# Kernel optimization log

Hardware: AMD Instinct MI355X
Metric: run time of the kernel (lower is better)

Reference implementation:

```python
import jax, jax.numpy as jnp
import numpy as np

NCE_T = 0.07   # opt.nce_T
EPS = 1e-8     # torch CosineSimilarity eps
DIAG_FILL = -10.0

N, D = 8192, 256

def setup_inputs() -> dict:
    key = jax.random.key(0)
    kq, kk = jax.random.split(key)
    feat_q = jax.random.normal(kq, (N, D), dtype=jnp.float32)
    feat_k = jax.random.normal(kk, (N, D), dtype=jnp.float32)
    return {"feat_q": feat_q, "feat_k": feat_k}

def reference(feat_q, feat_k):
    # feat_k is detached in the original
    feat_k = jax.lax.stop_gradient(feat_k)
    nq = jnp.linalg.norm(feat_q, axis=-1)            # [N]
    nk = jnp.linalg.norm(feat_k, axis=-1)            # [N]
    # positive cosine similarity (paired rows)
    l_pos = jnp.sum(feat_q * feat_k, axis=-1) / jnp.maximum(nq * nk, EPS)  # [N]
    # full N x N cosine similarity via GEMM (torch does a broadcasted version)
    sim = (feat_q @ feat_k.T) / jnp.maximum(nq[:, None] * nk[None, :], EPS)  # [N,N]
    # mask self-similarities with -10.0 BEFORE dividing by temperature
    diag = jnp.eye(sim.shape[0], dtype=bool)
    l_neg = jnp.where(diag, DIAG_FILL, sim)
    out = jnp.concatenate([l_pos[:, None], l_neg], axis=1) / NCE_T  # [N, N+1]
    # cross-entropy vs target class 0, reduction='none'
    loss = jax.scipy.special.logsumexp(out, axis=1) - out[:, 0]     # [N]
    return loss
```

## Files before the change

kernel.cpp:

```cpp
#include <hip/hip_runtime.h>
#include <stdint.h>
#include <math.h>

#define NROWS 8192
#define DDIM  256
#define BM    128
#define BN    128
#define GJ    8
#define COLS_PER_GROUP (NROWS / GJ)

constexpr float INV_T  = 1.0f / 0.07f;
constexpr float LOG2E  = 1.44269504f;
constexpr float K1     = INV_T * LOG2E;

typedef __bf16 bf16x8 __attribute__((ext_vector_type(8)));
typedef float  f32x4  __attribute__((ext_vector_type(4)));

__device__ __forceinline__ void async_copy16(const uint16_t* g, uint16_t* l) {
    __builtin_amdgcn_global_load_lds(
        (const __attribute__((address_space(1))) uint32_t*)g,
        (__attribute__((address_space(3))) uint32_t*)l, 16, 0, 0);
}

__device__ inline uint16_t f2bf(float f) {
    uint32_t u = __float_as_uint(f);
    u += 0x7fffu + ((u >> 16) & 1u);
    return (uint16_t)(u >> 16);
}

__global__ __launch_bounds__(256) void norm_convert_kernel(
    const float* __restrict__ fq, const float* __restrict__ fk,
    uint16_t* __restrict__ qb, uint16_t* __restrict__ kb)
{
    const int wave = threadIdx.x >> 6;
    const int lane = threadIdx.x & 63;
    const int row  = blockIdx.x * 4 + wave;

    const float* src; uint16_t* dstb;
    if (row < NROWS) {
        src = fq + (size_t)row * DDIM; dstb = qb + (size_t)row * DDIM;
    } else {
        int r = row - NROWS;
        src = fk + (size_t)r * DDIM; dstb = kb + (size_t)r * DDIM;
    }

    float4 v = ((const float4*)src)[lane];
    float ss = v.x*v.x + v.y*v.y + v.z*v.z + v.w*v.w;
    #pragma unroll
    for (int m = 1; m < 64; m <<= 1) ss += __shfl_xor(ss, m, 64);
    float r = rsqrtf(ss);

    ushort4 o;
    o.x = f2bf(v.x * r); o.y = f2bf(v.y * r); o.z = f2bf(v.z * r); o.w = f2bf(v.w * r);
    ((ushort4*)dstb)[lane] = o;
}

__global__ __launch_bounds__(256, 2) void nce_main_kernel(
    const uint16_t* __restrict__ qb, const uint16_t* __restrict__ kb,
    float* __restrict__ lpT, float* __restrict__ gpl)
{
    __shared__ __align__(16) uint16_t lds_q[BM * DDIM];
    __shared__ __align__(16) uint16_t lds_k[2 * BN * 32];

    const int tid    = threadIdx.x;
    const int wave   = tid >> 6;
    const int lane   = tid & 63;
    const int quad   = lane >> 4;
    const int lanelo = lane & 15;
    const int wr     = wave >> 1;
    const int wc     = wave & 1;
    const int rowBase      = blockIdx.x * BM;
    const int colGroupBase = blockIdx.y * COLS_PER_GROUP;

    #pragma unroll
    for (int i = 0; i < 16; ++i) {
        int S   = (wave * 16 + i) * 64 + lane;
        int row = S >> 5;
        int ch  = (S & 31) ^ (row & 31);
        async_copy16(qb + (size_t)(rowBase + row) * DDIM + ch * 8,
                     lds_q + (size_t)(wave * 16 + i) * 512);
    }

    int kS0   = wave * 128 + lane;
    int krow0 = kS0 >> 2;
    int kch0  = (lane & 3) ^ (krow0 & 3);
    int krow1 = (kS0 + 64) >> 2;
    int kch1  = (lane & 3) ^ (krow1 & 3);
    const uint16_t* kbase0 = kb + (size_t)(colGroupBase + krow0) * DDIM + kch0 * 8;
    const uint16_t* kbase1 = kb + (size_t)(colGroupBase + krow1) * DDIM + kch1 * 8;
    uint16_t* kl0 = lds_k + wave * 1024;

    async_copy16(kbase0, kl0);
    async_copy16(kbase1, kl0 + 512);
    __syncthreads();

    int rq[4], rq31[4];
    #pragma unroll
    for (int mt = 0; mt < 4; ++mt) {
        rq[mt]   = wr * 64 + mt * 16 + lanelo;
        rq31[mt] = rq[mt] & 31;
    }
    int bvoff[4];
    #pragma unroll
    for (int nt = 0; nt < 4; ++nt) {
        int rk = wc * 64 + nt * 16 + lanelo;
        bvoff[nt] = rk * 32 + (quad ^ (rk & 3)) * 8;
    }

    float l_run[16];
    #pragma unroll
    for (int i = 0; i < 16; ++i) l_run[i] = 0.f;

    for (int jt = 0; jt < 8; ++jt) {
        const int colT = colGroupBase + jt * BN;

        f32x4 acc[4][4];
        #pragma unroll
        for (int mt = 0; mt < 4; ++mt)
            #pragma unroll
            for (int nt = 0; nt < 4; ++nt)
                acc[mt][nt] = (f32x4){0.f, 0.f, 0.f, 0.f};

        #pragma unroll
        for (int kk = 0; kk < 8; ++kk) {
            const int p    = (jt << 3) + kk;
            const int buf  = p & 1;
            const int nbuf = buf ^ 1;

            if (p < 63) {
                int np  = p + 1;
                int off = ((np >> 3) << 15) + ((np & 7) << 5);
                uint16_t* ld = lds_k + nbuf * 4096 + wave * 1024;
                async_copy16(kbase0 + off, ld);
                async_copy16(kbase1 + off, ld + 512);
            }

            bf16x8 av[4], bv[4];
            #pragma unroll
            for (int mt = 0; mt < 4; ++mt) {
                int chp = ((kk << 2) + quad) ^ rq31[mt];
                av[mt] = *(const bf16x8*)&lds_q[rq[mt] * 256 + chp * 8];
            }
            #pragma unroll
            for (int nt = 0; nt < 4; ++nt)
                bv[nt] = *(const bf16x8*)&lds_k[buf * 4096 + bvoff[nt]];
            #pragma unroll
            for (int mt = 0; mt < 4; ++mt)
                #pragma unroll
                for (int nt = 0; nt < 4; ++nt)
                    acc[mt][nt] = __builtin_amdgcn_mfma_f32_16x16x32_bf16(av[mt], bv[nt], acc[mt][nt], 0, 0, 0);

            __syncthreads();
        }

        int gcol[4];
        #pragma unroll
        for (int nt = 0; nt < 4; ++nt) gcol[nt] = colT + wc * 64 + nt * 16 + lanelo;
        #pragma unroll
        for (int mt = 0; mt < 4; ++mt) {
            #pragma unroll
            for (int rg = 0; rg < 4; ++rg) {
                int grow = rowBase + wr * 64 + mt * 16 + quad * 4 + rg;
                float s = 0.f;
                #pragma unroll
                for (int nt = 0; nt < 4; ++nt) {
                    float a = acc[mt][nt][rg];
                    float e = exp2f(fmaf(a, K1, -K1));
                    if (grow == gcol[nt]) { lpT[grow] = a * INV_T; e = 0.f; }
                    s += e;
                }
                l_run[mt * 4 + rg] += s;
            }
        }
    }

    #pragma unroll
    for (int i = 0; i < 16; ++i) {
        float v = l_run[i];
        v += __shfl_xor(v, 1, 64);
        v += __shfl_xor(v, 2, 64);
        v += __shfl_xor(v, 4, 64);
        v += __shfl_xor(v, 8, 64);
        l_run[i] = v;
    }
    float* pl = (float*)lds_k;
    if (lanelo == 0) {
        #pragma unroll
        for (int mt = 0; mt < 4; ++mt)
            #pragma unroll
            for (int rg = 0; rg < 4; ++rg) {
                int lr = wr * 64 + mt * 16 + quad * 4 + rg;
                pl[wc * 128 + lr] = l_run[mt * 4 + rg];
            }
    }
    __syncthreads();
    if (tid < 128) {
        float L = pl[tid] + pl[128 + tid];
        gpl[(size_t)blockIdx.y * NROWS + rowBase + tid] = L;
    }
}

__global__ __launch_bounds__(256) void finalize_kernel(
    const float* __restrict__ gpl, const float* __restrict__ lpT,
    float* __restrict__ out)
{
    int t = blockIdx.x * 256 + threadIdx.x;
    if (t >= NROWS) return;
    float L = 0.f;
    #pragma unroll
    for (int g = 0; g < GJ; ++g) L += gpl[g * NROWS + t];
    float lp = lpT[t];
    L += __expf(lp - INV_T);
    out[t] = INV_T + __logf(L) - lp;
}

extern "C" void kernel_launch(void* const* d_in, const int* in_sizes, int n_in,
                              void* d_out, int out_size, void* d_ws, size_t ws_size,
                              hipStream_t stream) {
    const float* fq = (const float*)d_in[0];
    const float* fk = (const float*)d_in[1];
    char* ws = (char*)d_ws;
    uint16_t* qb  = (uint16_t*)(ws);
    uint16_t* kb  = (uint16_t*)(ws + 4194304);
    float*    lpT = (float*)(ws + 8388608);
    float*    gpl = (float*)(ws + 8421376);

    norm_convert_kernel<<<(2 * NROWS) / 4, 256, 0, stream>>>(fq, fk, qb, kb);
    dim3 grid(NROWS / BM, GJ);
    nce_main_kernel<<<grid, 256, 0, stream>>>(qb, kb, lpT, gpl);
    finalize_kernel<<<NROWS / 256, 256, 0, stream>>>(gpl, lpT, (float*)d_out);
}
```

Baseline: 112.3 us.

## Keep Q tile in registers and deepen K pipeline to four LDS buffers

The Q operand fragments are loaded once from global memory into registers (128 VGPRs per lane) instead of being staged through a 64KB LDS tile and re-read every k-step. The K stream now uses a 4-buffer ring with a prefetch distance of 3, and a vmcnt wait plus a raw barrier replace the full __syncthreads. MFMA sections are also wrapped with s_setprio. This frees LDS, removes the A-side LDS reads and allows deeper latency hiding, but raises register pressure, which could cause spills or lower occupancy under launch_bounds(256,2).

```diff
diff --git a/kernel.cpp b/kernel.cpp
--- a/kernel.cpp
+++ b/kernel.cpp
@@ -59,8 +59,7 @@
     const uint16_t* __restrict__ qb, const uint16_t* __restrict__ kb,
     float* __restrict__ lpT, float* __restrict__ gpl)
 {
-    __shared__ __align__(16) uint16_t lds_q[BM * DDIM];
-    __shared__ __align__(16) uint16_t lds_k[2 * BN * 32];
+    __shared__ __align__(16) uint16_t lds_k[4 * BN * 32];
 
     const int tid    = threadIdx.x;
     const int wave   = tid >> 6;
@@ -72,13 +71,14 @@
     const int rowBase      = blockIdx.x * BM;
     const int colGroupBase = blockIdx.y * COLS_PER_GROUP;
 
-    #pragma unroll
-    for (int i = 0; i < 16; ++i) {
-        int S   = (wave * 16 + i) * 64 + lane;
-        int row = S >> 5;
-        int ch  = (S & 31) ^ (row & 31);
-        async_copy16(qb + (size_t)(rowBase + row) * DDIM + ch * 8,
-                     lds_q + (size_t)(wave * 16 + i) * 512);
+    bf16x8 aq[4][8];
+    #pragma unroll
+    for (int mt = 0; mt < 4; ++mt) {
+        const uint16_t* qrow =
+            qb + (size_t)(rowBase + wr * 64 + mt * 16 + lanelo) * DDIM + quad * 8;
+        #pragma unroll
+        for (int kk = 0; kk < 8; ++kk)
+            aq[mt][kk] = *(const bf16x8*)(qrow + kk * 32);
     }
 
     int kS0   = wave * 128 + lane;
@@ -88,18 +88,14 @@
     int kch1  = (lane & 3) ^ (krow1 & 3);
     const uint16_t* kbase0 = kb + (size_t)(colGroupBase + krow0) * DDIM + kch0 * 8;
     const uint16_t* kbase1 = kb + (size_t)(colGroupBase + krow1) * DDIM + kch1 * 8;
-    uint16_t* kl0 = lds_k + wave * 1024;
-
-    async_copy16(kbase0, kl0);
-    async_copy16(kbase1, kl0 + 512);
-    __syncthreads();
-
-    int rq[4], rq31[4];
-    #pragma unroll
-    for (int mt = 0; mt < 4; ++mt) {
-        rq[mt]   = wr * 64 + mt * 16 + lanelo;
-        rq31[mt] = rq[mt] & 31;
-    }
+
+    #pragma unroll
+    for (int p = 0; p < 3; ++p) {
+        uint16_t* ld = lds_k + (p << 12) + (wave << 10);
+        async_copy16(kbase0 + (p << 5), ld);
+        async_copy16(kbase1 + (p << 5), ld + 512);
+    }
+
     int bvoff[4];
     #pragma unroll
     for (int nt = 0; nt < 4; ++nt) {
@@ -123,34 +119,34 @@
 
         #pragma unroll
         for (int kk = 0; kk < 8; ++kk) {
-            const int p    = (jt << 3) + kk;
-            const int buf  = p & 1;
-            const int nbuf = buf ^ 1;
-
-            if (p < 63) {
-                int np  = p + 1;
-                int off = ((np >> 3) << 15) + ((np & 7) << 5);
-                uint16_t* ld = lds_k + nbuf * 4096 + wave * 1024;
+            const int p = (jt << 3) + kk;
+
+            asm volatile("s_waitcnt vmcnt(4)" ::: "memory");
+            __builtin_amdgcn_s_barrier();
+
+            {
+                const int np  = p + 3;
+                const int npm = np & 63;
+                const int off = ((npm >> 3) << 15) + ((npm & 7) << 5);
+                uint16_t* ld = lds_k + ((np & 3) << 12) + (wave << 10);
                 async_copy16(kbase0 + off, ld);
                 async_copy16(kbase1 + off, ld + 512);
             }
 
-            bf16x8 av[4], bv[4];
-            #pragma unroll
-            for (int mt = 0; mt < 4; ++mt) {
-                int chp = ((kk << 2) + quad) ^ rq31[mt];
-                av[mt] = *(const bf16x8*)&lds_q[rq[mt] * 256 + chp * 8];
-            }
+            bf16x8 bv[4];
+            const int bufo = (p & 3) << 12;
             #pragma unroll
             for (int nt = 0; nt < 4; ++nt)
-                bv[nt] = *(const bf16x8*)&lds_k[buf * 4096 + bvoff[nt]];
+                bv[nt] = *(const bf16x8*)&lds_k[bufo + bvoff[nt]];
+
+            __builtin_amdgcn_s_setprio(1);
             #pragma unroll
             for (int mt = 0; mt < 4; ++mt)
                 #pragma unroll
                 for (int nt = 0; nt < 4; ++nt)
-                    acc[mt][nt] = __builtin_amdgcn_mfma_f32_16x16x32_bf16(av[mt], bv[nt], acc[mt][nt], 0, 0, 0);
-
-            __syncthreads();
+                    acc[mt][nt] = __builtin_amdgcn_mfma_f32_16x16x32_bf16(
+                        aq[mt][kk], bv[nt], acc[mt][nt], 0, 0, 0);
+            __builtin_amdgcn_s_setprio(0);
         }
 
         int gcol[4];
@@ -183,6 +179,9 @@
         v += __shfl_xor(v, 8, 64);
         l_run[i] = v;
     }
+
+    __syncthreads();
+
     float* pl = (float*)lds_k;
     if (lanelo == 0) {
         #pragma unroll
```

Result: slower. 116.5 us (+3.7%).

## Fuse normalize, GEMM and finalize into one cooperative kernel with grid syncs

Applied to the files above, without the earlier changes.

Replaces the three-kernel sequence with a single cooperative launch: the blocks first normalize and convert rows to bf16, sync the whole grid, run the GEMM/logsumexp phase, sync again, then finalize the per-row loss. The aim is to remove two kernel launch gaps and their tail effects. It also changes the LDS XOR swizzle for the K tile to use (row>>1)&3, to cut bank conflicts on the B-fragment reads. It keeps the old three-kernel path as a fallback if the cooperative launch fails. Grid syncs add a barrier cost, and the 512-block grid must fit co-resident at two blocks per CU.

```diff
diff --git a/kernel.cpp b/kernel.cpp
--- a/kernel.cpp
+++ b/kernel.cpp
@@ -1,4 +1,5 @@
 #include <hip/hip_runtime.h>
+#include <hip/hip_cooperative_groups.h>
 #include <stdint.h>
 #include <math.h>
 
@@ -16,6 +17,8 @@
 typedef __bf16 bf16x8 __attribute__((ext_vector_type(8)));
 typedef float  f32x4  __attribute__((ext_vector_type(4)));
 
+namespace cg = cooperative_groups;
+
 __device__ __forceinline__ void async_copy16(const uint16_t* g, uint16_t* l) {
     __builtin_amdgcn_global_load_lds(
         (const __attribute__((address_space(1))) uint32_t*)g,
@@ -28,40 +31,22 @@
     return (uint16_t)(u >> 16);
 }
 
-__global__ __launch_bounds__(256) void norm_convert_kernel(
-    const float* __restrict__ fq, const float* __restrict__ fk,
-    uint16_t* __restrict__ qb, uint16_t* __restrict__ kb)
-{
-    const int wave = threadIdx.x >> 6;
-    const int lane = threadIdx.x & 63;
-    const int row  = blockIdx.x * 4 + wave;
-
-    const float* src; uint16_t* dstb;
-    if (row < NROWS) {
-        src = fq + (size_t)row * DDIM; dstb = qb + (size_t)row * DDIM;
-    } else {
-        int r = row - NROWS;
-        src = fk + (size_t)r * DDIM; dstb = kb + (size_t)r * DDIM;
-    }
-
+__device__ __forceinline__ void norm_row(const float* src, uint16_t* dstb, int lane) {
     float4 v = ((const float4*)src)[lane];
     float ss = v.x*v.x + v.y*v.y + v.z*v.z + v.w*v.w;
     #pragma unroll
     for (int m = 1; m < 64; m <<= 1) ss += __shfl_xor(ss, m, 64);
     float r = rsqrtf(ss);
-
     ushort4 o;
     o.x = f2bf(v.x * r); o.y = f2bf(v.y * r); o.z = f2bf(v.z * r); o.w = f2bf(v.w * r);
     ((ushort4*)dstb)[lane] = o;
 }
 
-__global__ __launch_bounds__(256, 2) void nce_main_kernel(
+__device__ __forceinline__ void gemm_phase(
     const uint16_t* __restrict__ qb, const uint16_t* __restrict__ kb,
-    float* __restrict__ lpT, float* __restrict__ gpl)
-{
-    __shared__ __align__(16) uint16_t lds_q[BM * DDIM];
-    __shared__ __align__(16) uint16_t lds_k[2 * BN * 32];
-
+    float* __restrict__ lpT, float* __restrict__ gpl,
+    uint16_t* lds_q, uint16_t* lds_k, int bx, int by)
+{
     const int tid    = threadIdx.x;
     const int wave   = tid >> 6;
     const int lane   = tid & 63;
@@ -69,8 +54,8 @@
     const int lanelo = lane & 15;
     const int wr     = wave >> 1;
     const int wc     = wave & 1;
-    const int rowBase      = blockIdx.x * BM;
-    const int colGroupBase = blockIdx.y * COLS_PER_GROUP;
+    const int rowBase      = bx * BM;
+    const int colGroupBase = by * COLS_PER_GROUP;
 
     #pragma unroll
     for (int i = 0; i < 16; ++i) {
@@ -83,9 +68,9 @@
 
     int kS0   = wave * 128 + lane;
     int krow0 = kS0 >> 2;
-    int kch0  = (lane & 3) ^ (krow0 & 3);
+    int kch0  = (lane & 3) ^ ((krow0 >> 1) & 3);
     int krow1 = (kS0 + 64) >> 2;
-    int kch1  = (lane & 3) ^ (krow1 & 3);
+    int kch1  = (lane & 3) ^ ((krow1 >> 1) & 3);
     const uint16_t* kbase0 = kb + (size_t)(colGroupBase + krow0) * DDIM + kch0 * 8;
     const uint16_t* kbase1 = kb + (size_t)(colGroupBase + krow1) * DDIM + kch1 * 8;
     uint16_t* kl0 = lds_k + wave * 1024;
@@ -104,7 +89,7 @@
     #pragma unroll
     for (int nt = 0; nt < 4; ++nt) {
         int rk = wc * 64 + nt * 16 + lanelo;
-        bvoff[nt] = rk * 32 + (quad ^ (rk & 3)) * 8;
+        bvoff[nt] = rk * 32 + (quad ^ ((lanelo >> 1) & 3)) * 8;
     }
 
     float l_run[16];
@@ -196,8 +181,71 @@
     __syncthreads();
     if (tid < 128) {
         float L = pl[tid] + pl[128 + tid];
-        gpl[(size_t)blockIdx.y * NROWS + rowBase + tid] = L;
-    }
+        gpl[(size_t)by * NROWS + rowBase + tid] = L;
+    }
+}
+
+__global__ __launch_bounds__(256, 2) void fused_kernel(
+    const float* __restrict__ fq, const float* __restrict__ fk,
+    uint16_t* __restrict__ qb, uint16_t* __restrict__ kb,
+    float* __restrict__ lpT, float* __restrict__ gpl,
+    float* __restrict__ out)
+{
+    __shared__ __align__(16) uint16_t lds_q[BM * DDIM];
+    __shared__ __align__(16) uint16_t lds_k[2 * BN * 32];
+
+    const int wave = threadIdx.x >> 6;
+    const int lane = threadIdx.x & 63;
+    const int flat = blockIdx.y * gridDim.x + blockIdx.x;
+
+    #pragma unroll
+    for (int i = 0; i < 8; ++i) {
+        int row = flat * 32 + wave * 8 + i;
+        if (row < NROWS) norm_row(fq + (size_t)row * DDIM, qb + (size_t)row * DDIM, lane);
+        else {
+            int r = row - NROWS;
+            norm_row(fk + (size_t)r * DDIM, kb + (size_t)r * DDIM, lane);
+        }
+    }
+
+    cg::this_grid().sync();
+
+    gemm_phase(qb, kb, lpT, gpl, lds_q, lds_k, blockIdx.x, blockIdx.y);
+
+    cg::this_grid().sync();
+
+    int t = flat * 16 + threadIdx.x;
+    if (threadIdx.x < 16) {
+        float L = 0.f;
+        #pragma unroll
+        for (int g = 0; g < GJ; ++g) L += gpl[g * NROWS + t];
+        float lp = lpT[t];
+        L += __expf(lp - INV_T);
+        out[t] = INV_T + __logf(L) - lp;
+    }
+}
+
+__global__ __launch_bounds__(256) void norm_convert_kernel(
+    const float* __restrict__ fq, const float* __restrict__ fk,
+    uint16_t* __restrict__ qb, uint16_t* __restrict__ kb)
+{
+    const int wave = threadIdx.x >> 6;
+    const int lane = threadIdx.x & 63;
+    const int row  = blockIdx.x * 4 + wave;
+    if (row < NROWS) norm_row(fq + (size_t)row * DDIM, qb + (size_t)row * DDIM, lane);
+    else {
+        int r = row - NROWS;
+        norm_row(fk + (size_t)r * DDIM, kb + (size_t)r * DDIM, lane);
+    }
+}
+
+__global__ __launch_bounds__(256, 2) void nce_main_kernel(
+    const uint16_t* __restrict__ qb, const uint16_t* __restrict__ kb,
+    float* __restrict__ lpT, float* __restrict__ gpl)
+{
+    __shared__ __align__(16) uint16_t lds_q[BM * DDIM];
+    __shared__ __align__(16) uint16_t lds_k[2 * BN * 32];
+    gemm_phase(qb, kb, lpT, gpl, lds_q, lds_k, blockIdx.x, blockIdx.y);
 }
 
 __global__ __launch_bounds__(256) void finalize_kernel(
@@ -224,9 +272,17 @@
     uint16_t* kb  = (uint16_t*)(ws + 4194304);
     float*    lpT = (float*)(ws + 8388608);
     float*    gpl = (float*)(ws + 8421376);
-
-    norm_convert_kernel<<<(2 * NROWS) / 4, 256, 0, stream>>>(fq, fk, qb, kb);
-    dim3 grid(NROWS / BM, GJ);
-    nce_main_kernel<<<grid, 256, 0, stream>>>(qb, kb, lpT, gpl);
-    finalize_kernel<<<NROWS / 256, 256, 0, stream>>>(gpl, lpT, (float*)d_out);
-}
+    float*    outp = (float*)d_out;
+
+    void* kargs[] = { (void*)&fq, (void*)&fk, (void*)&qb, (void*)&kb,
+                      (void*)&lpT, (void*)&gpl, (void*)&outp };
+    hipError_t e = hipLaunchCooperativeKernel(
+        (const void*)fused_kernel, dim3(NROWS / BM, GJ), dim3(256), kargs, 0, stream);
+    if (e != hipSuccess) {
+        (void)hipGetLastError();
+        norm_convert_kernel<<<(2 * NROWS) / 4, 256, 0, stream>>>(fq, fk, qb, kb);
+        dim3 grid(NROWS / BM, GJ);
+        nce_main_kernel<<<grid, 256, 0, stream>>>(qb, kb, lpT, gpl);
+        finalize_kernel<<<NROWS / 256, 256, 0, stream>>>(gpl, lpT, outp);
+    }
+}
```

Measured after the change: 236.2 us. 2.1x slower.
